# Kernel tuning notes

Hardware: AMD Instinct MI355X
Metric: run time of the kernel (lower is better)

Reference implementation:

```python
import jax, jax.numpy as jnp
import numpy as np

N = 50000
E = 800000
DIN = 64
DOUT = 64
H = 4
C = DOUT // H
EPS = 1e-5


def setup_inputs() -> dict:
    key = jax.random.key(0)
    ks = jax.random.split(key, 40)
    inp = {}
    inp["x"] = jax.random.normal(ks[0], (N, DIN), jnp.float32)
    inp["edge_index"] = jax.random.randint(ks[1], (2, E), 0, N, dtype=jnp.int32)
    inp["edge_weight"] = jax.random.uniform(ks[2], (E,), jnp.float32)
    inp["edge_attr"] = jax.random.normal(ks[3], (E, 1), jnp.float32)
    k = 4
    for i in range(2):
        din = DIN if i == 0 else DOUT
        s = din ** -0.5
        inp[f"gcn_w{i}"] = jax.random.normal(ks[k], (din, DOUT), jnp.float32) * s; k += 1
        inp[f"gcn_b{i}"] = jnp.zeros((DOUT,), jnp.float32)
        inp[f"res_w{i}"] = jax.random.normal(ks[k], (din, DOUT), jnp.float32) * s; k += 1
        inp[f"res_b{i}"] = jnp.zeros((DOUT,), jnp.float32)
        inp[f"ln_g{i}"] = jnp.ones((DOUT,), jnp.float32)
        inp[f"ln_b{i}"] = jnp.zeros((DOUT,), jnp.float32)
        sg = DOUT ** -0.5
        inp[f"gat_w{i}"] = jax.random.normal(ks[k], (DOUT, H * C), jnp.float32) * sg; k += 1
        inp[f"gat_b{i}"] = jnp.zeros((H * C,), jnp.float32)
        inp[f"att_src{i}"] = jax.random.normal(ks[k], (H, C), jnp.float32) * (C ** -0.5); k += 1
        inp[f"att_dst{i}"] = jax.random.normal(ks[k], (H, C), jnp.float32) * (C ** -0.5); k += 1
        inp[f"att_e{i}"] = jax.random.normal(ks[k], (H, C), jnp.float32) * (C ** -0.5); k += 1
        inp[f"ew_w{i}"] = jax.random.normal(ks[k], (1, H * C), jnp.float32); k += 1
    return inp


def _gcn(x, src0, dst0, ew, W, b):
    n = x.shape[0]
    sl = jnp.arange(n, dtype=src0.dtype)
    src = jnp.concatenate([src0, sl])
    dst = jnp.concatenate([dst0, sl])
    w = jnp.concatenate([ew, jnp.ones((n,), ew.dtype)])  # self-loop weight 1
    deg = jax.ops.segment_sum(w, dst, num_segments=n)
    dinv = jnp.where(deg > 0, jax.lax.rsqrt(deg), 0.0)
    norm = dinv[src] * w * dinv[dst]
    h = x @ W  # [n, DOUT]
    out = jax.ops.segment_sum(h[src] * norm[:, None], dst, num_segments=n)
    return out + b


def _gat(x, src0, dst0, ea, W, b, a_src, a_dst, a_e, We):
    n = x.shape[0]
    sl = jnp.arange(n, dtype=src0.dtype)
    src = jnp.concatenate([src0, sl])
    dst = jnp.concatenate([dst0, sl])
    loop_attr = jnp.broadcast_to(ea.mean(axis=0, keepdims=True), (n, ea.shape[1]))
    ea2 = jnp.concatenate([ea, loop_attr], axis=0)  # fill_value='mean'
    xl = (x @ W).reshape(n, H, C)
    a_s = (xl * a_src).sum(-1)  # [n,H]
    a_d = (xl * a_dst).sum(-1)
    a_ee = ((ea2 @ We).reshape(-1, H, C) * a_e).sum(-1)  # [E2,H]
    alpha = jax.nn.leaky_relu(a_s[src] + a_d[dst] + a_ee, 0.2)
    m = jax.ops.segment_max(alpha, dst, num_segments=n)
    e = jnp.exp(alpha - m[dst])
    s = jax.ops.segment_sum(e, dst, num_segments=n)
    alpha = e / (s[dst] + 1e-16)
    out = jax.ops.segment_sum(xl[src] * alpha[:, :, None], dst, num_segments=n)
    return out.reshape(n, H * C) + b


def _ln(x, g, b):
    mu = x.mean(-1, keepdims=True)
    v = ((x - mu) ** 2).mean(-1, keepdims=True)
    return (x - mu) * jax.lax.rsqrt(v + EPS) * g + b


def reference(x, edge_index, edge_weight, edge_attr,
              gcn_w0, gcn_b0, res_w0, res_b0, ln_g0, ln_b0,
              gat_w0, gat_b0, att_src0, att_dst0, att_e0, ew_w0,
              gcn_w1, gcn_b1, res_w1, res_b1, ln_g1, ln_b1,
              gat_w1, gat_b1, att_src1, att_dst1, att_e1, ew_w1):
    src0, dst0 = edge_index[0], edge_index[1]
    layers = [
        (gcn_w0, gcn_b0, res_w0, res_b0, ln_g0, ln_b0, gat_w0, gat_b0, att_src0, att_dst0, att_e0, ew_w0),
        (gcn_w1, gcn_b1, res_w1, res_b1, ln_g1, ln_b1, gat_w1, gat_b1, att_src1, att_dst1, att_e1, ew_w1),
    ]
    for (gw, gb, rw, rb, lg, lb, Wg, bg, a_s, a_d, a_e, We) in layers:
        residual = x @ rw + rb
        x = jax.nn.silu(_gcn(x, src0, dst0, edge_weight, gw, gb)) + residual
        x = _ln(x, lg, lb)
        x = jax.nn.silu(_gat(x, src0, dst0, edge_attr, Wg, bg, a_s, a_d, a_e, We)) + x
    return x  # down_sample=False -> Identity
```

## Files before the change

### kernel.cpp

```cpp
#include <hip/hip_runtime.h>
#include <hip/hip_fp16.h>

#define NN 50000
#define NE 800000
#define D 64
#define EPS 1e-5f
#define NT 3125
#define NB1 250
#define EPB 3200
#define NBIN 196
#define STOT 49152
#define SBLK 192
#define CAP 5888

typedef unsigned short ushort_t;
typedef unsigned int uint_t;
typedef __attribute__((ext_vector_type(8))) short bf16x8;
typedef __attribute__((ext_vector_type(4))) float f32x4;

__device__ __forceinline__ float wave_sum64(float v) {
#pragma unroll
  for (int m = 1; m <= 32; m <<= 1) v += __shfl_xor(v, m, 64);
  return v;
}
__device__ __forceinline__ float half_sum32(float v) {
#pragma unroll
  for (int m = 1; m <= 16; m <<= 1) v += __shfl_xor(v, m, 64);
  return v;
}
__device__ __forceinline__ float group_sum16(float v) {
#pragma unroll
  for (int m = 1; m <= 8; m <<= 1) v += __shfl_xor(v, m, 64);
  return v;
}
__device__ __forceinline__ float silu_f(float v) { return v / (1.f + __expf(-v)); }
__device__ __forceinline__ float lrelu_f(float v) { return v >= 0.f ? v : 0.2f * v; }
__device__ __forceinline__ ushort_t f2b(float x) {
  unsigned u = __float_as_uint(x);
  return (ushort_t)((u + 0x7FFFu + ((u >> 16) & 1u)) >> 16);
}
__device__ __forceinline__ float b2f(ushort_t u) {
  return __uint_as_float(((unsigned)u) << 16);
}
__device__ __forceinline__ float b2f_lo(uint_t u) {
  return __uint_as_float(u << 16);
}
__device__ __forceinline__ float b2f_hi(uint_t u) {
  return __uint_as_float(u & 0xFFFF0000u);
}
__device__ __forceinline__ ushort_t f2h(float x) {
  return __half_as_ushort(__float2half_rn(x));
}
__device__ __forceinline__ float h2f(unsigned u) {
  return __half2float(__ushort_as_half((ushort_t)(u & 0xFFFFu)));
}
__device__ __forceinline__ float sel4(float a, float b, float c, float d, int h) {
  float ab = (h & 1) ? b : a;
  float cd = (h & 1) ? d : c;
  return (h & 2) ? cd : ab;
}
__device__ __forceinline__ bf16x8 pack8(float4 a, float4 b) {
  bf16x8 r;
  r[0] = (short)f2b(a.x); r[1] = (short)f2b(a.y);
  r[2] = (short)f2b(a.z); r[3] = (short)f2b(a.w);
  r[4] = (short)f2b(b.x); r[5] = (short)f2b(b.y);
  r[6] = (short)f2b(b.z); r[7] = (short)f2b(b.w);
  return r;
}

__global__ void __launch_bounds__(256) k_hist(const int* __restrict__ ei,
                                              int* __restrict__ histG) {
  __shared__ int h[NBIN];
  int blk = blockIdx.x;
  for (int j = threadIdx.x; j < NBIN; j += 256) h[j] = 0;
  __syncthreads();
  int e0 = blk * EPB;
  for (int e = e0 + threadIdx.x; e < e0 + EPB; e += 256)
    atomicAdd(&h[ei[NE + e] >> 8], 1);
  __syncthreads();
  for (int j = threadIdx.x; j < NBIN; j += 256) histG[j * NB1 + blk] = h[j];
}

__global__ void __launch_bounds__(256) k_scanA(
    int* __restrict__ histG, int* __restrict__ bsum, float* __restrict__ scal,
    const float* __restrict__ Wg0, const float* __restrict__ Wg1,
    const float* __restrict__ W11, const float* __restrict__ W21,
    const float* __restrict__ We0, const float* __restrict__ ae0,
    const float* __restrict__ We1, const float* __restrict__ ae1,
    ushort_t* __restrict__ wg16, ushort_t* __restrict__ wd16,
    float* __restrict__ wea2) {
  if (blockIdx.x == SBLK) {
    int tid = threadIdx.x;
    for (int t = tid; t < 1024; t += 256) scal[t] = 0.f;
    for (int e = tid; e < 4096; e += 256) {
      int f = e >> 9, r = e & 511;
      int lane = r >> 3, j = r & 7;
      int s = (f >> 2) & 1, t = f & 3;
      int k = s * 32 + (lane >> 4) * 8 + j;
      int n = t * 16 + (lane & 15);
      wg16[e] = f2b(Wg0[k * D + n]);
      wg16[4096 + e] = f2b(Wg1[k * D + n]);
    }
    for (int e = tid; e < 8192; e += 256) {
      int f = e >> 9, r = e & 511;
      int lane = r >> 3, j = r & 7;
      int m = f >> 3, s = (f >> 2) & 1, t = f & 3;
      int k = s * 32 + (lane >> 4) * 8 + j;
      int n = t * 16 + (lane & 15);
      const float* Wm = m ? W21 : W11;
      wd16[e] = f2b(Wm[k * D + n]);
    }
    if (tid < 64) {
      float v = group_sum16(We0[tid] * ae0[tid]);
      if ((tid & 15) == 0) wea2[tid >> 4] = v;
    } else if (tid < 128) {
      int c = tid - 64;
      float v = group_sum16(We1[c] * ae1[c]);
      if ((c & 15) == 0) wea2[4 + (c >> 4)] = v;
    }
    return;
  }
  __shared__ int sm[256];
  int j = threadIdx.x;
  int i = blockIdx.x * 256 + j;
  const int TOT = NBIN * NB1;
  int v = (i < TOT) ? histG[i] : 0;
  sm[j] = v;
  __syncthreads();
  for (int off = 1; off < 256; off <<= 1) {
    int t = (j >= off) ? sm[j - off] : 0;
    __syncthreads();
    sm[j] += t;
    __syncthreads();
  }
  if (i < TOT) histG[i] = sm[j] - v;
  if (j == 255) bsum[blockIdx.x] = sm[255];
}

__global__ void __launch_bounds__(256) k_part(
    const int* __restrict__ ei, const float* __restrict__ ew,
    const float* __restrict__ ea, const int* __restrict__ histG,
    const int* __restrict__ bsum,
    uint2* __restrict__ rectmp, float* __restrict__ scal) {
  __shared__ int cur[NBIN];
  __shared__ int pex[256];
  int blk = blockIdx.x;
  int t = threadIdx.x;
  int v0 = (t < SBLK) ? bsum[t] : 0;
  pex[t] = v0;
  __syncthreads();
  for (int off = 1; off < 256; off <<= 1) {
    int u = (t >= off) ? pex[t - off] : 0;
    __syncthreads();
    pex[t] += u;
    __syncthreads();
  }
  int ex0 = pex[t] - v0;
  __syncthreads();
  pex[t] = ex0;
  __syncthreads();
  for (int j = t; j < NBIN; j += 256) {
    int idx = j * NB1 + blk;
    cur[j] = histG[idx] + pex[idx >> 8];
  }
  __syncthreads();
  int e0 = blk * EPB;
  float asum = 0.f;
  for (int e = e0 + t; e < e0 + EPB; e += 256) {
    int src = ei[e];
    int dst = ei[NE + e];
    float w = ew[e];
    float a = ea[e];
    asum += a;
    int slot = atomicAdd(&cur[dst >> 8], 1);
    uint2 r;
    r.x = (uint_t)(src & 0xFFFF) | ((uint_t)f2h(w) << 16);
    r.y = (uint_t)(dst & 0xFF) | ((uint_t)f2h(a) << 16);
    rectmp[slot] = r;
  }
  float s = wave_sum64(asum);
  if ((t & 63) == 0) {
    int slot = (blk * 4 + (t >> 6)) & 63;
    atomicAdd(&scal[(size_t)slot * 16], s);
  }
}

__global__ void __launch_bounds__(256) k_sfing(
    const uint2* __restrict__ rectmp, const int* __restrict__ histG,
    const int* __restrict__ bsum,
    uint_t* __restrict__ recw, uint_t* __restrict__ reca, int* __restrict__ rs,
    float* __restrict__ dinv, float* __restrict__ scal,
    const float* __restrict__ x, const float* __restrict__ W1,
    const float* __restrict__ W2, const float* __restrict__ b2,
    ushort_t* __restrict__ out1, float* __restrict__ out2) {
  __shared__ __align__(16) char smem[4096 + CAP * 8];
  int t = threadIdx.x;
  if (blockIdx.x >= NBIN) {
    ushort_t* wf = (ushort_t*)smem;
    for (int e = t; e < 8192; e += 256) {
      int f = e >> 9, r = e & 511;
      int lane = r >> 3, j = r & 7;
      int m = f >> 3, s = (f >> 2) & 1, tt = f & 3;
      int k = s * 32 + (lane >> 4) * 8 + j;
      int n = tt * 16 + (lane & 15);
      const float* Wm = m ? W2 : W1;
      wf[e] = f2b(Wm[k * D + n]);
    }
    __syncthreads();
    int tile = (blockIdx.x - NBIN) * 4 + (t >> 6);
    if (tile >= NT) return;
    int l = t & 63;
    int q = l >> 4, cn = l & 15;
    const float* xr = x + ((size_t)tile * 16 + cn) * D + q * 8;
    float4 xa = *(const float4*)xr;
    float4 xb = *(const float4*)(xr + 4);
    float4 xc = *(const float4*)(xr + 32);
    float4 xd = *(const float4*)(xr + 36);
    bf16x8 a0 = pack8(xa, xb), a1 = pack8(xc, xd);
    f32x4 acc1[4], acc2[4];
#pragma unroll
    for (int tt = 0; tt < 4; ++tt) {
      bf16x8 b10 = *(const bf16x8*)&wf[(0 * 8 + 0 * 4 + tt) * 512 + l * 8];
      bf16x8 b11 = *(const bf16x8*)&wf[(0 * 8 + 1 * 4 + tt) * 512 + l * 8];
      bf16x8 b20 = *(const bf16x8*)&wf[(1 * 8 + 0 * 4 + tt) * 512 + l * 8];
      bf16x8 b21 = *(const bf16x8*)&wf[(1 * 8 + 1 * 4 + tt) * 512 + l * 8];
      f32x4 z = {0.f, 0.f, 0.f, 0.f};
      acc1[tt] = __builtin_amdgcn_mfma_f32_16x16x32_bf16(a0, b10, z, 0, 0, 0);
      acc1[tt] = __builtin_amdgcn_mfma_f32_16x16x32_bf16(a1, b11, acc1[tt], 0, 0, 0);
      acc2[tt] = __builtin_amdgcn_mfma_f32_16x16x32_bf16(a0, b20, z, 0, 0, 0);
      acc2[tt] = __builtin_amdgcn_mfma_f32_16x16x32_bf16(a1, b21, acc2[tt], 0, 0, 0);
    }
#pragma unroll
    for (int tt = 0; tt < 4; ++tt) {
      float bb = b2[tt * 16 + cn];
#pragma unroll
      for (int r = 0; r < 4; ++r) {
        size_t row = (size_t)tile * 16 + q * 4 + r;
        out1[row * D + tt * 16 + cn] = f2b(acc1[tt][r]);
        out2[row * D + tt * 16 + cn] = acc2[tt][r] + bb;
      }
    }
    return;
  }
  int* cnt = (int*)smem;
  int* sc  = cnt + 256;
  int* cur = sc + 256;
  float* wsum = (float*)(cur + 256);
  uint2* lrec = (uint2*)(smem + 4096);
  int b = blockIdx.x;
  int v0 = (t < SBLK) ? bsum[t] : 0;
  sc[t] = v0;
  __syncthreads();
  for (int off = 1; off < 256; off <<= 1) {
    int u = (t >= off) ? sc[t - off] : 0;
    __syncthreads();
    sc[t] += u;
    __syncthreads();
  }
  int ex0 = sc[t] - v0;
  __syncthreads();
  sc[t] = ex0;
  __syncthreads();
  int i0 = b * NB1;
  int lo = histG[i0] + sc[i0 >> 8];
  int hi;
  if (b == NBIN - 1) {
    hi = NE;
  } else {
    int i1 = (b + 1) * NB1;
    hi = histG[i1] + sc[i1 >> 8];
  }
  __syncthreads();
  cnt[t] = 0;
  wsum[t] = 0.f;
  __syncthreads();
  int nc = min(hi - lo, CAP);
  for (int e = t; e < nc; e += 256) lrec[e] = rectmp[lo + e];
  __syncthreads();
  for (int e = t; e < nc; e += 256)
    atomicAdd(&cnt[lrec[e].y & 0xFFu], 1);
  for (int e = lo + CAP + t; e < hi; e += 256)
    atomicAdd(&cnt[rectmp[e].y & 0xFFu], 1);
  __syncthreads();
  int v = cnt[t];
  sc[t] = v;
  __syncthreads();
  for (int off = 1; off < 256; off <<= 1) {
    int u = (t >= off) ? sc[t - off] : 0;
    __syncthreads();
    sc[t] += u;
    __syncthreads();
  }
  int ex = sc[t] - v;
  int node = b * 256 + t;
  if (node < NN) rs[node] = lo + ex;
  if (b == NBIN - 1 && t == 0) rs[NN] = NE;
  cur[t] = lo + ex;
  __syncthreads();
  for (int e = t; e < nc; e += 256) {
    uint2 r = lrec[e];
    int dl = (int)(r.y & 0xFFu);
    int slot = atomicAdd(&cur[dl], 1);
    atomicAdd(&wsum[dl], h2f(r.x >> 16));
    uint_t src = r.x & 0xFFFFu;
    recw[slot] = r.x;
    reca[slot] = src | (r.y & 0xFFFF0000u);
  }
  for (int e = lo + CAP + t; e < hi; e += 256) {
    uint2 r = rectmp[e];
    int dl = (int)(r.y & 0xFFu);
    int slot = atomicAdd(&cur[dl], 1);
    atomicAdd(&wsum[dl], h2f(r.x >> 16));
    uint_t src = r.x & 0xFFFFu;
    recw[slot] = r.x;
    reca[slot] = src | (r.y & 0xFFFF0000u);
  }
  __syncthreads();
  if (node < NN) dinv[node] = rsqrtf(1.f + wsum[t]);
  if (b == 0 && t == 0) {
    float s = 0.f;
    for (int j = 0; j < 64; ++j) s += scal[(size_t)j * 16];
    scal[1] = s / (float)NE;
  }
}

__global__ void __launch_bounds__(256) k_gcn_gat(
    const ushort_t* __restrict__ h16, const float* __restrict__ res,
    const float* __restrict__ dinv, const int* __restrict__ rs,
    const uint_t* __restrict__ recw,
    const float* __restrict__ gb, const float* __restrict__ lg,
    const float* __restrict__ lb,
    const ushort_t* __restrict__ wg, const float* __restrict__ att_src,
    const float* __restrict__ att_dst,
    float* __restrict__ x2, ushort_t* __restrict__ xl,
    float* __restrict__ a_s, float* __restrict__ a_d) {
  __shared__ int ss[4][64];
  __shared__ float swt[4][64];
  __shared__ __align__(16) ushort_t xt[16][72];
  int w = threadIdx.x >> 6;
  int l = threadIdx.x & 63;
  int base = blockIdx.x * 8;
  int half = l >> 5, c = l & 31;
  int iA = base + 2 * w;
  int iB = iA + 1;
  int i = iA + half;
  float di = dinv[i];
  uint_t u0 = *(const uint_t*)&h16[(size_t)i * D + 2 * c];
  float dii = di * di;
  float acc0 = dii * b2f_lo(u0);
  float acc1 = dii * b2f_hi(u0);
  int kA = rs[iA], kA1 = rs[iA + 1];
  int kB = rs[iB], kB1 = rs[iB + 1];
  int sbase = half * 32;
  while (kA < kA1 || kB < kB1) {
    int cntA = min(32, kA1 - kA);
    int cntB = min(32, kB1 - kB);
    int myk = half ? kB : kA;
    int mycnt = half ? cntB : cntA;
    int src = 0; float wn = 0.f;
    if (c < mycnt) {
      uint_t r = recw[(size_t)(myk + c)];
      src = (int)(r & 0xFFFFu);
      wn = dinv[src] * h2f(r >> 16) * di;
    }
    ss[w][l] = src;
    swt[w][l] = wn;
    int nm = max(cntA, cntB);
    int j = 0;
    for (; j + 4 <= nm; j += 4) {
      int4 s4 = *(const int4*)&ss[w][sbase + j];
      float4 w4 = *(const float4*)&swt[w][sbase + j];
      uint_t ua = *(const uint_t*)&h16[(size_t)s4.x * D + 2 * c];
      uint_t ub = *(const uint_t*)&h16[(size_t)s4.y * D + 2 * c];
      uint_t uc = *(const uint_t*)&h16[(size_t)s4.z * D + 2 * c];
      uint_t ud = *(const uint_t*)&h16[(size_t)s4.w * D + 2 * c];
      acc0 = fmaf(w4.x, b2f_lo(ua), acc0); acc1 = fmaf(w4.x, b2f_hi(ua), acc1);
      acc0 = fmaf(w4.y, b2f_lo(ub), acc0); acc1 = fmaf(w4.y, b2f_hi(ub), acc1);
      acc0 = fmaf(w4.z, b2f_lo(uc), acc0); acc1 = fmaf(w4.z, b2f_hi(uc), acc1);
      acc0 = fmaf(w4.w, b2f_lo(ud), acc0); acc1 = fmaf(w4.w, b2f_hi(ud), acc1);
    }
    for (; j < nm; ++j) {
      int s1 = ss[w][sbase + j];
      float w1 = swt[w][sbase + j];
      uint_t u = *(const uint_t*)&h16[(size_t)s1 * D + 2 * c];
      acc0 = fmaf(w1, b2f_lo(u), acc0);
      acc1 = fmaf(w1, b2f_hi(u), acc1);
    }
    kA += cntA; kB += cntB;
  }
  float2 gb2 = *(const float2*)&gb[2 * c];
  float2 lg2 = *(const float2*)&lg[2 * c];
  float2 lb2 = *(const float2*)&lb[2 * c];
  float2 rs2 = *(const float2*)&res[(size_t)i * D + 2 * c];
  float x0 = silu_f(acc0 + gb2.x) + rs2.x;
  float x1 = silu_f(acc1 + gb2.y) + rs2.y;
  float mu = half_sum32(x0 + x1) * (1.f / 64.f);
  float d0 = x0 - mu, d1 = x1 - mu;
  float var = half_sum32(d0 * d0 + d1 * d1) * (1.f / 64.f);
  float rinv = rsqrtf(var + EPS);
  float o0 = d0 * rinv * lg2.x + lb2.x;
  float o1 = d1 * rinv * lg2.y + lb2.y;
  float2 o2; o2.x = o0; o2.y = o1;
  *(float2*)&x2[(size_t)i * D + 2 * c] = o2;
  uint_t pk = (uint_t)f2b(o0) | ((uint_t)f2b(o1) << 16);
  *(uint_t*)&xt[2 * w + half][2 * c] = pk;
  {
    ushort_t* xz = &xt[8][0];
    for (int e = threadIdx.x; e < 8 * 72; e += 256) xz[e] = 0;
  }
  __syncthreads();
  int t = w;
  int q = l >> 4, cn = l & 15;
  bf16x8 a0 = *(const bf16x8*)&xt[cn][q * 8];
  bf16x8 a1 = *(const bf16x8*)&xt[cn][q * 8 + 32];
  bf16x8 b0 = *(const bf16x8*)&wg[(size_t)((0 * 4 + t) * 512 + l * 8)];
  bf16x8 b1 = *(const bf16x8*)&wg[(size_t)((1 * 4 + t) * 512 + l * 8)];
  f32x4 z = {0.f, 0.f, 0.f, 0.f};
  f32x4 acc = __builtin_amdgcn_mfma_f32_16x16x32_bf16(a0, b0, z, 0, 0, 0);
  acc = __builtin_amdgcn_mfma_f32_16x16x32_bf16(a1, b1, acc, 0, 0, 0);
  if (q < 2) {
    float av = att_src[t * 16 + cn];
    float dv = att_dst[t * 16 + cn];
#pragma unroll
    for (int r = 0; r < 4; ++r) {
      size_t row = (size_t)base + q * 4 + r;
      xl[row * D + t * 16 + cn] = f2b(acc[r]);
      float vs = group_sum16(acc[r] * av);
      float vd = group_sum16(acc[r] * dv);
      if (cn == 0) {
        a_s[row * 4 + t] = vs;
        a_d[row * 4 + t] = vd;
      }
    }
  }
}

template <int FUSE>
__global__ void __launch_bounds__(256) k_gat_fin(
    const ushort_t* __restrict__ xl16, const float* __restrict__ x2,
    const float* __restrict__ a_s, const float* __restrict__ a_d,
    const int* __restrict__ rs, const uint_t* __restrict__ reca,
    const float* __restrict__ wea, const float* __restrict__ scal,
    const float* __restrict__ bg,
    const ushort_t* __restrict__ wd, const float* __restrict__ b2,
    ushort_t* __restrict__ out1, float* __restrict__ out2,
    float* __restrict__ xout) {
  __shared__ int ss[4][64];
  __shared__ float el[4][4][68];
  __shared__ __align__(16) ushort_t xt[16][72];
  int w = threadIdx.x >> 6;
  int l = threadIdx.x & 63;
  int base = blockIdx.x * 8;
  int half = l >> 5, c = l & 31;
  int iA = base + 2 * w;
  int iB = iA + 1;
  int i = iA + half;
  int hh = c >> 3;
  float4 wv4 = *(const float4*)wea;
  float mean_attr = scal[1];
  float we_h = sel4(wv4.x, wv4.y, wv4.z, wv4.w, hh);
  float ad_h = a_d[(size_t)i * 4 + hh];
  float as_i = a_s[(size_t)i * 4 + hh];
  float eS = __expf(lrelu_f(as_i + ad_h + mean_attr * we_h));
  float s = eS;
  uint_t u0 = *(const uint_t*)&xl16[(size_t)i * D + 2 * c];
  float acc0 = eS * b2f_lo(u0);
  float acc1 = eS * b2f_hi(u0);
  float4 ad4 = *(const float4*)(a_d + (size_t)i * 4);
  int kA = rs[iA], kA1 = rs[iA + 1];
  int kB = rs[iB], kB1 = rs[iB + 1];
  int sbase = half * 32;
  while (kA < kA1 || kB < kB1) {
    int cntA = min(32, kA1 - kA);
    int cntB = min(32, kB1 - kB);
    int myk = half ? kB : kA;
    int mycnt = half ? cntB : cntA;
    int src = 0;
    float e0v = 0.f, e1v = 0.f, e2v = 0.f, e3v = 0.f;
    if (c < mycnt) {
      uint_t r = reca[(size_t)(myk + c)];
      src = (int)(r & 0xFFFFu);
      float ea = h2f(r >> 16);
      float4 as4 = *(const float4*)(a_s + (size_t)src * 4);
      e0v = __expf(lrelu_f(as4.x + fmaf(ea, wv4.x, ad4.x)));
      e1v = __expf(lrelu_f(as4.y + fmaf(ea, wv4.y, ad4.y)));
      e2v = __expf(lrelu_f(as4.z + fmaf(ea, wv4.z, ad4.z)));
      e3v = __expf(lrelu_f(as4.w + fmaf(ea, wv4.w, ad4.w)));
    }
    ss[w][l] = src;
    el[w][0][l] = e0v;
    el[w][1][l] = e1v;
    el[w][2][l] = e2v;
    el[w][3][l] = e3v;
    int nm = max(cntA, cntB);
    int j = 0;
    for (; j + 4 <= nm; j += 4) {
      int4 s4 = *(const int4*)&ss[w][sbase + j];
      float4 e4 = *(const float4*)&el[w][hh][sbase + j];
      uint_t ua = *(const uint_t*)&xl16[(size_t)s4.x * D + 2 * c];
      uint_t ub = *(const uint_t*)&xl16[(size_t)s4.y * D + 2 * c];
      uint_t uc = *(const uint_t*)&xl16[(size_t)s4.z * D + 2 * c];
      uint_t ud = *(const uint_t*)&xl16[(size_t)s4.w * D + 2 * c];
      acc0 = fmaf(e4.x, b2f_lo(ua), acc0); acc1 = fmaf(e4.x, b2f_hi(ua), acc1);
      acc0 = fmaf(e4.y, b2f_lo(ub), acc0); acc1 = fmaf(e4.y, b2f_hi(ub), acc1);
      acc0 = fmaf(e4.z, b2f_lo(uc), acc0); acc1 = fmaf(e4.z, b2f_hi(uc), acc1);
      acc0 = fmaf(e4.w, b2f_lo(ud), acc0); acc1 = fmaf(e4.w, b2f_hi(ud), acc1);
      s += (e4.x + e4.y) + (e4.z + e4.w);
    }
    for (; j < nm; ++j) {
      int s1 = ss[w][sbase + j];
      float e1 = el[w][hh][sbase + j];
      uint_t u = *(const uint_t*)&xl16[(size_t)s1 * D + 2 * c];
      acc0 = fmaf(e1, b2f_lo(u), acc0);
      acc1 = fmaf(e1, b2f_hi(u), acc1);
      s += e1;
    }
    kA += cntA; kB += cntB;
  }
  float2 bg2 = *(const float2*)&bg[2 * c];
  float rcp = 1.f / (s + 1e-16f);
  float o0 = acc0 * rcp + bg2.x;
  float o1 = acc1 * rcp + bg2.y;
  float2 x22 = *(const float2*)&x2[(size_t)i * D + 2 * c];
  float v0 = silu_f(o0) + x22.x;
  float v1 = silu_f(o1) + x22.y;
  if (FUSE) {
    uint_t pk = (uint_t)f2b(v0) | ((uint_t)f2b(v1) << 16);
    *(uint_t*)&xt[2 * w + half][2 * c] = pk;
    {
      ushort_t* xz = &xt[8][0];
      for (int e = threadIdx.x; e < 8 * 72; e += 256) xz[e] = 0;
    }
    __syncthreads();
    int t = w;
    int q = l >> 4, cn = l & 15;
    bf16x8 a0 = *(const bf16x8*)&xt[cn][q * 8];
    bf16x8 a1 = *(const bf16x8*)&xt[cn][q * 8 + 32];
#pragma unroll
    for (int m = 0; m < 2; ++m) {
      bf16x8 b0 = *(const bf16x8*)&wd[(size_t)((m * 8 + 0 * 4 + t) * 512 + l * 8)];
      bf16x8 b1 = *(const bf16x8*)&wd[(size_t)((m * 8 + 1 * 4 + t) * 512 + l * 8)];
      f32x4 z = {0.f, 0.f, 0.f, 0.f};
      f32x4 acc = __builtin_amdgcn_mfma_f32_16x16x32_bf16(a0, b0, z, 0, 0, 0);
      acc = __builtin_amdgcn_mfma_f32_16x16x32_bf16(a1, b1, acc, 0, 0, 0);
      if (q < 2) {
        float bb = (m == 1) ? b2[t * 16 + cn] : 0.f;
#pragma unroll
        for (int r = 0; r < 4; ++r) {
          size_t row = (size_t)base + q * 4 + r;
          if (m == 0)
            out1[row * D + t * 16 + cn] = f2b(acc[r]);
          else
            out2[row * D + t * 16 + cn] = acc[r] + bb;
        }
      }
    }
  } else {
    float2 v2; v2.x = v0; v2.y = v1;
    *(float2*)&xout[(size_t)i * D + 2 * c] = v2;
  }
}


extern "C" void kernel_launch(void* const* d_in, const int* in_sizes, int n_in,
                              void* d_out, int out_size, void* d_ws, size_t ws_size,
                              hipStream_t stream) {
  (void)in_sizes; (void)n_in; (void)out_size; (void)ws_size;
  const float* x  = (const float*)d_in[0];
  const int*   ei = (const int*)d_in[1];
  const float* ew = (const float*)d_in[2];
  const float* ea = (const float*)d_in[3];
  const float* P[2][12];
  for (int l = 0; l < 2; ++l)
    for (int j = 0; j < 12; ++j) P[l][j] = (const float*)d_in[4 + l * 12 + j];

  float* W = (float*)d_ws;
  const size_t o_rs    = 0;
  const size_t o_dinv  = o_rs + NN + 16;
  const size_t o_wea   = o_dinv + NN;
  const size_t o_scal  = o_wea + 16;
  const size_t o_bsum  = o_scal + 1024;
  const size_t o_hist  = o_bsum + 256;
  const size_t o_recw  = o_hist + STOT;
  const size_t o_reca  = o_recw + NE;
  const size_t o_rtmp  = o_reca + NE;
  const size_t o_h16   = o_rtmp + (size_t)NE * 2;
  const size_t o_xl16  = o_h16 + (size_t)NN * D / 2;
  const size_t o_res   = o_xl16 + (size_t)NN * D / 2;
  const size_t o_x2    = o_res + (size_t)NN * D;
  const size_t o_as    = o_x2 + (size_t)NN * D;
  const size_t o_ad    = o_as + (size_t)NN * 4;
  const size_t o_wg16  = o_ad + (size_t)NN * 4;
  const size_t o_wd16  = o_wg16 + 4096;

  int*      rs    = (int*)(W + o_rs);
  float*    dinv  = W + o_dinv;
  float*    wea2  = W + o_wea;
  float*    scal  = W + o_scal;
  int*      bsum  = (int*)(W + o_bsum);
  int*      histG = (int*)(W + o_hist);
  uint_t*   recw  = (uint_t*)(W + o_recw);
  uint_t*   reca  = (uint_t*)(W + o_reca);
  uint2*    rtmp  = (uint2*)(W + o_rtmp);
  ushort_t* h16   = (ushort_t*)(W + o_h16);
  ushort_t* xl16  = (ushort_t*)(W + o_xl16);
  float*    resb  = W + o_res;
  float*    x2b   = W + o_x2;
  float*    asb   = W + o_as;
  float*    adb   = W + o_ad;
  ushort_t* wg16  = (ushort_t*)(W + o_wg16);
  ushort_t* wd16  = (ushort_t*)(W + o_wd16);

  const int B = 256;
  const int gSf = NBIN + (NT + 3) / 4;
  const int gN2 = NN / 8;

  k_hist<<<NB1, B, 0, stream>>>(ei, histG);
  k_scanA<<<SBLK + 1, B, 0, stream>>>(histG, bsum, scal,
                                      P[0][6], P[1][6], P[1][0], P[1][2],
                                      P[0][11], P[0][10], P[1][11], P[1][10],
                                      wg16, wd16, wea2);
  k_part<<<NB1, B, 0, stream>>>(ei, ew, ea, histG, bsum, rtmp, scal);
  k_sfing<<<gSf, B, 0, stream>>>(rtmp, histG, bsum, recw, reca, rs, dinv, scal,
                                 x, P[0][0], P[0][2], P[0][3], h16, resb);

  k_gcn_gat<<<gN2, B, 0, stream>>>(h16, resb, dinv, rs, recw,
                                   P[0][1], P[0][4], P[0][5],
                                   wg16, P[0][8], P[0][9],
                                   x2b, xl16, asb, adb);
  k_gat_fin<1><<<gN2, B, 0, stream>>>(xl16, x2b, asb, adb, rs, reca,
                                      wea2, scal, P[0][7],
                                      wd16, P[1][3], h16, resb, nullptr);
  k_gcn_gat<<<gN2, B, 0, stream>>>(h16, resb, dinv, rs, recw,
                                   P[1][1], P[1][4], P[1][5],
                                   wg16 + 4096, P[1][8], P[1][9],
                                   x2b, xl16, asb, adb);
  k_gat_fin<0><<<gN2, B, 0, stream>>>(xl16, x2b, asb, adb, rs, reca,
                                      wea2 + 4, scal, P[1][7],
                                      nullptr, nullptr, nullptr, nullptr,
                                      (float*)d_out);
}
```

Before: 277.2 us.

## Split edge gathers across two 16-lane groups with 8-byte loads, cache GCN norms

The GCN and GAT aggregation loops now have each 32-lane half-wave split into two 16-lane groups. Each group handles alternate edges and gathers 4 bf16 features per lane with 8-byte loads, and the two partial sums are combined with a shuffle at the end. This doubles the edges in flight per wave and widens each gather, aiming to hide irregular-gather latency better. Layer 0 also writes per-edge GCN normalisation weights into a new buffer that layer 1 reads back, skipping the dinv[src] gather. Source attention scores are additionally stored as fp16 to halve the per-edge gather size, at the cost of a small loss of precision.

```diff
diff --git a/kernel.cpp b/kernel.cpp
--- a/kernel.cpp
+++ b/kernel.cpp
@@ -21,11 +21,6 @@
 __device__ __forceinline__ float wave_sum64(float v) {
 #pragma unroll
   for (int m = 1; m <= 32; m <<= 1) v += __shfl_xor(v, m, 64);
-  return v;
-}
-__device__ __forceinline__ float half_sum32(float v) {
-#pragma unroll
-  for (int m = 1; m <= 16; m <<= 1) v += __shfl_xor(v, m, 64);
   return v;
 }
 __device__ __forceinline__ float group_sum16(float v) {
@@ -324,86 +319,109 @@
   }
 }
 
+template <int LAYER>
 __global__ void __launch_bounds__(256) k_gcn_gat(
     const ushort_t* __restrict__ h16, const float* __restrict__ res,
     const float* __restrict__ dinv, const int* __restrict__ rs,
-    const uint_t* __restrict__ recw,
+    const uint_t* __restrict__ recw, float* __restrict__ normc,
     const float* __restrict__ gb, const float* __restrict__ lg,
     const float* __restrict__ lb,
     const ushort_t* __restrict__ wg, const float* __restrict__ att_src,
     const float* __restrict__ att_dst,
     float* __restrict__ x2, ushort_t* __restrict__ xl,
-    float* __restrict__ a_s, float* __restrict__ a_d) {
+    float* __restrict__ a_s, float* __restrict__ a_d,
+    ushort_t* __restrict__ asf16) {
   __shared__ int ss[4][64];
   __shared__ float swt[4][64];
   __shared__ __align__(16) ushort_t xt[16][72];
   int w = threadIdx.x >> 6;
   int l = threadIdx.x & 63;
   int base = blockIdx.x * 8;
-  int half = l >> 5, c = l & 31;
+  int half = l >> 5;
+  int p = (l >> 4) & 1;
+  int cc = l & 15;
+  int ce = l & 31;
   int iA = base + 2 * w;
   int iB = iA + 1;
   int i = iA + half;
   float di = dinv[i];
-  uint_t u0 = *(const uint_t*)&h16[(size_t)i * D + 2 * c];
-  float dii = di * di;
-  float acc0 = dii * b2f_lo(u0);
-  float acc1 = dii * b2f_hi(u0);
+  float dii = (p == 0) ? di * di : 0.f;
+  uint2 u0 = *(const uint2*)&h16[(size_t)i * D + 4 * cc];
+  float a0c = dii * b2f_lo(u0.x);
+  float a1c = dii * b2f_hi(u0.x);
+  float a2c = dii * b2f_lo(u0.y);
+  float a3c = dii * b2f_hi(u0.y);
   int kA = rs[iA], kA1 = rs[iA + 1];
   int kB = rs[iB], kB1 = rs[iB + 1];
   int sbase = half * 32;
+  int gbase = sbase + (p << 4);
   while (kA < kA1 || kB < kB1) {
     int cntA = min(32, kA1 - kA);
     int cntB = min(32, kB1 - kB);
     int myk = half ? kB : kA;
     int mycnt = half ? cntB : cntA;
     int src = 0; float wn = 0.f;
-    if (c < mycnt) {
-      uint_t r = recw[(size_t)(myk + c)];
+    if (ce < mycnt) {
+      uint_t r = recw[(size_t)(myk + ce)];
       src = (int)(r & 0xFFFFu);
-      wn = dinv[src] * h2f(r >> 16) * di;
-    }
-    ss[w][l] = src;
-    swt[w][l] = wn;
+      if (LAYER == 0) {
+        wn = dinv[src] * h2f(r >> 16) * di;
+        normc[(size_t)(myk + ce)] = wn;
+      } else {
+        wn = normc[(size_t)(myk + ce)];
+      }
+    }
+    int slot = sbase + ((ce & 1) << 4) + (ce >> 1);
+    ss[w][slot] = src;
+    swt[w][slot] = wn;
     int nm = max(cntA, cntB);
-    int j = 0;
-    for (; j + 4 <= nm; j += 4) {
-      int4 s4 = *(const int4*)&ss[w][sbase + j];
-      float4 w4 = *(const float4*)&swt[w][sbase + j];
-      uint_t ua = *(const uint_t*)&h16[(size_t)s4.x * D + 2 * c];
-      uint_t ub = *(const uint_t*)&h16[(size_t)s4.y * D + 2 * c];
-      uint_t uc = *(const uint_t*)&h16[(size_t)s4.z * D + 2 * c];
-      uint_t ud = *(const uint_t*)&h16[(size_t)s4.w * D + 2 * c];
-      acc0 = fmaf(w4.x, b2f_lo(ua), acc0); acc1 = fmaf(w4.x, b2f_hi(ua), acc1);
-      acc0 = fmaf(w4.y, b2f_lo(ub), acc0); acc1 = fmaf(w4.y, b2f_hi(ub), acc1);
-      acc0 = fmaf(w4.z, b2f_lo(uc), acc0); acc1 = fmaf(w4.z, b2f_hi(uc), acc1);
-      acc0 = fmaf(w4.w, b2f_lo(ud), acc0); acc1 = fmaf(w4.w, b2f_hi(ud), acc1);
-    }
-    for (; j < nm; ++j) {
-      int s1 = ss[w][sbase + j];
-      float w1 = swt[w][sbase + j];
-      uint_t u = *(const uint_t*)&h16[(size_t)s1 * D + 2 * c];
-      acc0 = fmaf(w1, b2f_lo(u), acc0);
-      acc1 = fmaf(w1, b2f_hi(u), acc1);
+    int npj = (nm + 1) >> 1;
+    for (int pj = 0; pj < npj; pj += 4) {
+      int4 s4 = *(const int4*)&ss[w][gbase + pj];
+      float4 w4 = *(const float4*)&swt[w][gbase + pj];
+      uint2 ua = *(const uint2*)&h16[(size_t)s4.x * D + 4 * cc];
+      uint2 ub = *(const uint2*)&h16[(size_t)s4.y * D + 4 * cc];
+      uint2 uc = *(const uint2*)&h16[(size_t)s4.z * D + 4 * cc];
+      uint2 ud = *(const uint2*)&h16[(size_t)s4.w * D + 4 * cc];
+      a0c = fmaf(w4.x, b2f_lo(ua.x), a0c); a1c = fmaf(w4.x, b2f_hi(ua.x), a1c);
+      a2c = fmaf(w4.x, b2f_lo(ua.y), a2c); a3c = fmaf(w4.x, b2f_hi(ua.y), a3c);
+      a0c = fmaf(w4.y, b2f_lo(ub.x), a0c); a1c = fmaf(w4.y, b2f_hi(ub.x), a1c);
+      a2c = fmaf(w4.y, b2f_lo(ub.y), a2c); a3c = fmaf(w4.y, b2f_hi(ub.y), a3c);
+      a0c = fmaf(w4.z, b2f_lo(uc.x), a0c); a1c = fmaf(w4.z, b2f_hi(uc.x), a1c);
+      a2c = fmaf(w4.z, b2f_lo(uc.y), a2c); a3c = fmaf(w4.z, b2f_hi(uc.y), a3c);
+      a0c = fmaf(w4.w, b2f_lo(ud.x), a0c); a1c = fmaf(w4.w, b2f_hi(ud.x), a1c);
+      a2c = fmaf(w4.w, b2f_lo(ud.y), a2c); a3c = fmaf(w4.w, b2f_hi(ud.y), a3c);
     }
     kA += cntA; kB += cntB;
   }
-  float2 gb2 = *(const float2*)&gb[2 * c];
-  float2 lg2 = *(const float2*)&lg[2 * c];
-  float2 lb2 = *(const float2*)&lb[2 * c];
-  float2 rs2 = *(const float2*)&res[(size_t)i * D + 2 * c];
-  float x0 = silu_f(acc0 + gb2.x) + rs2.x;
-  float x1 = silu_f(acc1 + gb2.y) + rs2.y;
-  float mu = half_sum32(x0 + x1) * (1.f / 64.f);
-  float d0 = x0 - mu, d1 = x1 - mu;
-  float var = half_sum32(d0 * d0 + d1 * d1) * (1.f / 64.f);
+  a0c += __shfl_xor(a0c, 16, 64);
+  a1c += __shfl_xor(a1c, 16, 64);
+  a2c += __shfl_xor(a2c, 16, 64);
+  a3c += __shfl_xor(a3c, 16, 64);
+  float4 gb4 = *(const float4*)&gb[4 * cc];
+  float4 lg4 = *(const float4*)&lg[4 * cc];
+  float4 lb4 = *(const float4*)&lb[4 * cc];
+  float4 rs4 = *(const float4*)&res[(size_t)i * D + 4 * cc];
+  float x0 = silu_f(a0c + gb4.x) + rs4.x;
+  float x1 = silu_f(a1c + gb4.y) + rs4.y;
+  float x2v = silu_f(a2c + gb4.z) + rs4.z;
+  float x3 = silu_f(a3c + gb4.w) + rs4.w;
+  float mu = group_sum16((x0 + x1) + (x2v + x3)) * (1.f / 64.f);
+  float d0 = x0 - mu, d1 = x1 - mu, d2 = x2v - mu, d3 = x3 - mu;
+  float var = group_sum16((d0 * d0 + d1 * d1) + (d2 * d2 + d3 * d3)) * (1.f / 64.f);
   float rinv = rsqrtf(var + EPS);
-  float o0 = d0 * rinv * lg2.x + lb2.x;
-  float o1 = d1 * rinv * lg2.y + lb2.y;
-  float2 o2; o2.x = o0; o2.y = o1;
-  *(float2*)&x2[(size_t)i * D + 2 * c] = o2;
-  uint_t pk = (uint_t)f2b(o0) | ((uint_t)f2b(o1) << 16);
-  *(uint_t*)&xt[2 * w + half][2 * c] = pk;
+  float o0 = d0 * rinv * lg4.x + lb4.x;
+  float o1 = d1 * rinv * lg4.y + lb4.y;
+  float o2 = d2 * rinv * lg4.z + lb4.z;
+  float o3 = d3 * rinv * lg4.w + lb4.w;
+  if (p == 0) {
+    float4 ov; ov.x = o0; ov.y = o1; ov.z = o2; ov.w = o3;
+    *(float4*)&x2[(size_t)i * D + 4 * cc] = ov;
+    uint2 pk;
+    pk.x = (uint_t)f2b(o0) | ((uint_t)f2b(o1) << 16);
+    pk.y = (uint_t)f2b(o2) | ((uint_t)f2b(o3) << 16);
+    *(uint2*)&xt[2 * w + half][4 * cc] = pk;
+  }
   {
     ushort_t* xz = &xt[8][0];
     for (int e = threadIdx.x; e < 8 * 72; e += 256) xz[e] = 0;
@@ -411,13 +429,13 @@
   __syncthreads();
   int t = w;
   int q = l >> 4, cn = l & 15;
-  bf16x8 a0 = *(const bf16x8*)&xt[cn][q * 8];
-  bf16x8 a1 = *(const bf16x8*)&xt[cn][q * 8 + 32];
-  bf16x8 b0 = *(const bf16x8*)&wg[(size_t)((0 * 4 + t) * 512 + l * 8)];
-  bf16x8 b1 = *(const bf16x8*)&wg[(size_t)((1 * 4 + t) * 512 + l * 8)];
+  bf16x8 fa0 = *(const bf16x8*)&xt[cn][q * 8];
+  bf16x8 fa1 = *(const bf16x8*)&xt[cn][q * 8 + 32];
+  bf16x8 fb0 = *(const bf16x8*)&wg[(size_t)((0 * 4 + t) * 512 + l * 8)];
+  bf16x8 fb1 = *(const bf16x8*)&wg[(size_t)((1 * 4 + t) * 512 + l * 8)];
   f32x4 z = {0.f, 0.f, 0.f, 0.f};
-  f32x4 acc = __builtin_amdgcn_mfma_f32_16x16x32_bf16(a0, b0, z, 0, 0, 0);
-  acc = __builtin_amdgcn_mfma_f32_16x16x32_bf16(a1, b1, acc, 0, 0, 0);
+  f32x4 acc = __builtin_amdgcn_mfma_f32_16x16x32_bf16(fa0, fb0, z, 0, 0, 0);
+  acc = __builtin_amdgcn_mfma_f32_16x16x32_bf16(fa1, fb1, acc, 0, 0, 0);
   if (q < 2) {
     float av = att_src[t * 16 + cn];
     float dv = att_dst[t * 16 + cn];
@@ -430,6 +448,7 @@
       if (cn == 0) {
         a_s[row * 4 + t] = vs;
         a_d[row * 4 + t] = vd;
+        asf16[row * 4 + t] = f2h(vs);
       }
     }
   }
@@ -439,6 +458,7 @@
 __global__ void __launch_bounds__(256) k_gat_fin(
     const ushort_t* __restrict__ xl16, const float* __restrict__ x2,
     const float* __restrict__ a_s, const float* __restrict__ a_d,
+    const ushort_t* __restrict__ asf16,
     const int* __restrict__ rs, const uint_t* __restrict__ reca,
     const float* __restrict__ wea, const float* __restrict__ scal,
     const float* __restrict__ bg,
@@ -451,25 +471,32 @@
   int w = threadIdx.x >> 6;
   int l = threadIdx.x & 63;
   int base = blockIdx.x * 8;
-  int half = l >> 5, c = l & 31;
+  int half = l >> 5;
+  int p = (l >> 4) & 1;
+  int cc = l & 15;
+  int ce = l & 31;
   int iA = base + 2 * w;
   int iB = iA + 1;
   int i = iA + half;
-  int hh = c >> 3;
+  int hh = cc >> 2;
   float4 wv4 = *(const float4*)wea;
   float mean_attr = scal[1];
   float we_h = sel4(wv4.x, wv4.y, wv4.z, wv4.w, hh);
   float ad_h = a_d[(size_t)i * 4 + hh];
   float as_i = a_s[(size_t)i * 4 + hh];
   float eS = __expf(lrelu_f(as_i + ad_h + mean_attr * we_h));
-  float s = eS;
-  uint_t u0 = *(const uint_t*)&xl16[(size_t)i * D + 2 * c];
-  float acc0 = eS * b2f_lo(u0);
-  float acc1 = eS * b2f_hi(u0);
+  float eSm = (p == 0) ? eS : 0.f;
+  float s = eSm;
+  uint2 u0 = *(const uint2*)&xl16[(size_t)i * D + 4 * cc];
+  float a0c = eSm * b2f_lo(u0.x);
+  float a1c = eSm * b2f_hi(u0.x);
+  float a2c = eSm * b2f_lo(u0.y);
+  float a3c = eSm * b2f_hi(u0.y);
   float4 ad4 = *(const float4*)(a_d + (size_t)i * 4);
   int kA = rs[iA], kA1 = rs[iA + 1];
   int kB = rs[iB], kB1 = rs[iB + 1];
   int sbase = half * 32;
+  int gbase = sbase + (p << 4);
   while (kA < kA1 || kB < kB1) {
     int cntA = min(32, kA1 - kA);
     int cntB = min(32, kB1 - kB);
@@ -477,56 +504,64 @@
     int mycnt = half ? cntB : cntA;
     int src = 0;
     float e0v = 0.f, e1v = 0.f, e2v = 0.f, e3v = 0.f;
-    if (c < mycnt) {
-      uint_t r = reca[(size_t)(myk + c)];
+    if (ce < mycnt) {
+      uint_t r = reca[(size_t)(myk + ce)];
       src = (int)(r & 0xFFFFu);
       float ea = h2f(r >> 16);
-      float4 as4 = *(const float4*)(a_s + (size_t)src * 4);
-      e0v = __expf(lrelu_f(as4.x + fmaf(ea, wv4.x, ad4.x)));
-      e1v = __expf(lrelu_f(as4.y + fmaf(ea, wv4.y, ad4.y)));
-      e2v = __expf(lrelu_f(as4.z + fmaf(ea, wv4.z, ad4.z)));
-      e3v = __expf(lrelu_f(as4.w + fmaf(ea, wv4.w, ad4.w)));
-    }
-    ss[w][l] = src;
-    el[w][0][l] = e0v;
-    el[w][1][l] = e1v;
-    el[w][2][l] = e2v;
-    el[w][3][l] = e3v;
+      uint2 au = *(const uint2*)&asf16[(size_t)src * 4];
+      float as0 = h2f(au.x), as1 = h2f(au.x >> 16);
+      float as2 = h2f(au.y), as3 = h2f(au.y >> 16);
+      e0v = __expf(lrelu_f(as0 + fmaf(ea, wv4.x, ad4.x)));
+      e1v = __expf(lrelu_f(as1 + fmaf(ea, wv4.y, ad4.y)));
+      e2v = __expf(lrelu_f(as2 + fmaf(ea, wv4.z, ad4.z)));
+      e3v = __expf(lrelu_f(as3 + fmaf(ea, wv4.w, ad4.w)));
+    }
+    int slot = sbase + ((ce & 1) << 4) + (ce >> 1);
+    ss[w][slot] = src;
+    el[w][0][slot] = e0v;
+    el[w][1][slot] = e1v;
+    el[w][2][slot] = e2v;
+    el[w][3][slot] = e3v;
     int nm = max(cntA, cntB);
-    int j = 0;
-    for (; j + 4 <= nm; j += 4) {
-      int4 s4 = *(const int4*)&ss[w][sbase + j];
-      float4 e4 = *(const float4*)&el[w][hh][sbase + j];
-      uint_t ua = *(const uint_t*)&xl16[(size_t)s4.x * D + 2 * c];
-      uint_t ub = *(const uint_t*)&xl16[(size_t)s4.y * D + 2 * c];
-      uint_t uc = *(const uint_t*)&xl16[(size_t)s4.z * D + 2 * c];
-      uint_t ud = *(const uint_t*)&xl16[(size_t)s4.w * D + 2 * c];
-      acc0 = fmaf(e4.x, b2f_lo(ua), acc0); acc1 = fmaf(e4.x, b2f_hi(ua), acc1);
-      acc0 = fmaf(e4.y, b2f_lo(ub), acc0); acc1 = fmaf(e4.y, b2f_hi(ub), acc1);
-      acc0 = fmaf(e4.z, b2f_lo(uc), acc0); acc1 = fmaf(e4.z, b2f_hi(uc), acc1);
-      acc0 = fmaf(e4.w, b2f_lo(ud), acc0); acc1 = fmaf(e4.w, b2f_hi(ud), acc1);
+    int npj = (nm + 1) >> 1;
+    for (int pj = 0; pj < npj; pj += 4) {
+      int4 s4 = *(const int4*)&ss[w][gbase + pj];
+      float4 e4 = *(const float4*)&el[w][hh][gbase + pj];
+      uint2 ua = *(const uint2*)&xl16[(size_t)s4.x * D + 4 * cc];
+      uint2 ub = *(const uint2*)&xl16[(size_t)s4.y * D + 4 * cc];
+      uint2 uc = *(const uint2*)&xl16[(size_t)s4.z * D + 4 * cc];
+      uint2 ud = *(const uint2*)&xl16[(size_t)s4.w * D + 4 * cc];
+      a0c = fmaf(e4.x, b2f_lo(ua.x), a0c); a1c = fmaf(e4.x, b2f_hi(ua.x), a1c);
+      a2c = fmaf(e4.x, b2f_lo(ua.y), a2c); a3c = fmaf(e4.x, b2f_hi(ua.y), a3c);
+      a0c = fmaf(e4.y, b2f_lo(ub.x), a0c); a1c = fmaf(e4.y, b2f_hi(ub.x), a1c);
+      a2c = fmaf(e4.y, b2f_lo(ub.y), a2c); a3c = fmaf(e4.y, b2f_hi(ub.y), a3c);
+      a0c = fmaf(e4.z, b2f_lo(uc.x), a0c); a1c = fmaf(e4.z, b2f_hi(uc.x), a1c);
+      a2c = fmaf(e4.z, b2f_lo(uc.y), a2c); a3c = fmaf(e4.z, b2f_hi(uc.y), a3c);
+      a0c = fmaf(e4.w, b2f_lo(ud.x), a0c); a1c = fmaf(e4.w, b2f_hi(ud.x), a1c);
+      a2c = fmaf(e4.w, b2f_lo(ud.y), a2c); a3c = fmaf(e4.w, b2f_hi(ud.y), a3c);
       s += (e4.x + e4.y) + (e4.z + e4.w);
     }
-    for (; j < nm; ++j) {
-      int s1 = ss[w][sbase + j];
-      float e1 = el[w][hh][sbase + j];
-      uint_t u = *(const uint_t*)&xl16[(size_t)s1 * D + 2 * c];
-      acc0 = fmaf(e1, b2f_lo(u), acc0);
-      acc1 = fmaf(e1, b2f_hi(u), acc1);
-      s += e1;
-    }
     kA += cntA; kB += cntB;
   }
-  float2 bg2 = *(const float2*)&bg[2 * c];
+  a0c += __shfl_xor(a0c, 16, 64);
+  a1c += __shfl_xor(a1c, 16, 64);
+  a2c += __shfl_xor(a2c, 16, 64);
+  a3c += __shfl_xor(a3c, 16, 64);
+  s += __shfl_xor(s, 16, 64);
+  float4 bg4 = *(const float4*)&bg[4 * cc];
   float rcp = 1.f / (s + 1e-16f);
-  float o0 = acc0 * rcp + bg2.x;
-  float o1 = acc1 * rcp + bg2.y;
-  float2 x22 = *(const float2*)&x2[(size_t)i * D + 2 * c];
-  float v0 = silu_f(o0) + x22.x;
-  float v1 = silu_f(o1) + x22.y;
+  float4 x24 = *(const float4*)&x2[(size_t)i * D + 4 * cc];
+  float v0 = silu_f(a0c * rcp + bg4.x) + x24.x;
+  float v1 = silu_f(a1c * rcp + bg4.y) + x24.y;
+  float v2 = silu_f(a2c * rcp + bg4.z) + x24.z;
+  float v3 = silu_f(a3c * rcp + bg4.w) + x24.w;
   if (FUSE) {
-    uint_t pk = (uint_t)f2b(v0) | ((uint_t)f2b(v1) << 16);
-    *(uint_t*)&xt[2 * w + half][2 * c] = pk;
+    if (p == 0) {
+      uint2 pk;
+      pk.x = (uint_t)f2b(v0) | ((uint_t)f2b(v1) << 16);
+      pk.y = (uint_t)f2b(v2) | ((uint_t)f2b(v3) << 16);
+      *(uint2*)&xt[2 * w + half][4 * cc] = pk;
+    }
     {
       ushort_t* xz = &xt[8][0];
       for (int e = threadIdx.x; e < 8 * 72; e += 256) xz[e] = 0;
@@ -534,15 +569,15 @@
     __syncthreads();
     int t = w;
     int q = l >> 4, cn = l & 15;
-    bf16x8 a0 = *(const bf16x8*)&xt[cn][q * 8];
-    bf16x8 a1 = *(const bf16x8*)&xt[cn][q * 8 + 32];
+    bf16x8 fa0 = *(const bf16x8*)&xt[cn][q * 8];
+    bf16x8 fa1 = *(const bf16x8*)&xt[cn][q * 8 + 32];
 #pragma unroll
     for (int m = 0; m < 2; ++m) {
-      bf16x8 b0 = *(const bf16x8*)&wd[(size_t)((m * 8 + 0 * 4 + t) * 512 + l * 8)];
-      bf16x8 b1 = *(const bf16x8*)&wd[(size_t)((m * 8 + 1 * 4 + t) * 512 + l * 8)];
+      bf16x8 fb0 = *(const bf16x8*)&wd[(size_t)((m * 8 + 0 * 4 + t) * 512 + l * 8)];
+      bf16x8 fb1 = *(const bf16x8*)&wd[(size_t)((m * 8 + 1 * 4 + t) * 512 + l * 8)];
       f32x4 z = {0.f, 0.f, 0.f, 0.f};
-      f32x4 acc = __builtin_amdgcn_mfma_f32_16x16x32_bf16(a0, b0, z, 0, 0, 0);
-      acc = __builtin_amdgcn_mfma_f32_16x16x32_bf16(a1, b1, acc, 0, 0, 0);
+      f32x4 acc = __builtin_amdgcn_mfma_f32_16x16x32_bf16(fa0, fb0, z, 0, 0, 0);
+      acc = __builtin_amdgcn_mfma_f32_16x16x32_bf16(fa1, fb1, acc, 0, 0, 0);
       if (q < 2) {
         float bb = (m == 1) ? b2[t * 16 + cn] : 0.f;
 #pragma unroll
@@ -556,8 +591,10 @@
       }
     }
   } else {
-    float2 v2; v2.x = v0; v2.y = v1;
-    *(float2*)&xout[(size_t)i * D + 2 * c] = v2;
+    if (p == 0) {
+      float4 vv; vv.x = v0; vv.y = v1; vv.z = v2; vv.w = v3;
+      *(float4*)&xout[(size_t)i * D + 4 * cc] = vv;
+    }
   }
 }
 
@@ -583,14 +620,16 @@
   const size_t o_hist  = o_bsum + 256;
   const size_t o_recw  = o_hist + STOT;
   const size_t o_reca  = o_recw + NE;
-  const size_t o_rtmp  = o_reca + NE;
+  const size_t o_norm  = o_reca + NE;
+  const size_t o_rtmp  = o_norm + NE;
   const size_t o_h16   = o_rtmp + (size_t)NE * 2;
   const size_t o_xl16  = o_h16 + (size_t)NN * D / 2;
   const size_t o_res   = o_xl16 + (size_t)NN * D / 2;
   const size_t o_x2    = o_res + (size_t)NN * D;
   const size_t o_as    = o_x2 + (size_t)NN * D;
   const size_t o_ad    = o_as + (size_t)NN * 4;
-  const size_t o_wg16  = o_ad + (size_t)NN * 4;
+  const size_t o_ash   = o_ad + (size_t)NN * 4;
+  const size_t o_wg16  = o_ash + (size_t)NN * 2;
   const size_t o_wd16  = o_wg16 + 4096;
 
   int*      rs    = (int*)(W + o_rs);
@@ -601,6 +640,7 @@
   int*      histG = (int*)(W + o_hist);
   uint_t*   recw  = (uint_t*)(W + o_recw);
   uint_t*   reca  = (uint_t*)(W + o_reca);
+  float*    normc = W + o_norm;
   uint2*    rtmp  = (uint2*)(W + o_rtmp);
   ushort_t* h16   = (ushort_t*)(W + o_h16);
   ushort_t* xl16  = (ushort_t*)(W + o_xl16);
@@ -608,6 +648,7 @@
   float*    x2b   = W + o_x2;
   float*    asb   = W + o_as;
   float*    adb   = W + o_ad;
+  ushort_t* ashb  = (ushort_t*)(W + o_ash);
   ushort_t* wg16  = (ushort_t*)(W + o_wg16);
   ushort_t* wd16  = (ushort_t*)(W + o_wd16);
 
@@ -624,18 +665,18 @@
   k_sfing<<<gSf, B, 0, stream>>>(rtmp, histG, bsum, recw, reca, rs, dinv, scal,
                                  x, P[0][0], P[0][2], P[0][3], h16, resb);
 
-  k_gcn_gat<<<gN2, B, 0, stream>>>(h16, resb, dinv, rs, recw,
-                                   P[0][1], P[0][4], P[0][5],
-                                   wg16, P[0][8], P[0][9],
-                                   x2b, xl16, asb, adb);
-  k_gat_fin<1><<<gN2, B, 0, stream>>>(xl16, x2b, asb, adb, rs, reca,
+  k_gcn_gat<0><<<gN2, B, 0, stream>>>(h16, resb, dinv, rs, recw, normc,
+                                      P[0][1], P[0][4], P[0][5],
+                                      wg16, P[0][8], P[0][9],
+                                      x2b, xl16, asb, adb, ashb);
+  k_gat_fin<1><<<gN2, B, 0, stream>>>(xl16, x2b, asb, adb, ashb, rs, reca,
                                       wea2, scal, P[0][7],
                                       wd16, P[1][3], h16, resb, nullptr);
-  k_gcn_gat<<<gN2, B, 0, stream>>>(h16, resb, dinv, rs, recw,
-                                   P[1][1], P[1][4], P[1][5],
-                                   wg16 + 4096, P[1][8], P[1][9],
-                                   x2b, xl16, asb, adb);
-  k_gat_fin<0><<<gN2, B, 0, stream>>>(xl16, x2b, asb, adb, rs, reca,
+  k_gcn_gat<1><<<gN2, B, 0, stream>>>(h16, resb, dinv, rs, recw, normc,
+                                      P[1][1], P[1][4], P[1][5],
+                                      wg16 + 4096, P[1][8], P[1][9],
+                                      x2b, xl16, asb, adb, ashb);
+  k_gat_fin<0><<<gN2, B, 0, stream>>>(xl16, x2b, asb, adb, ashb, rs, reca,
                                       wea2 + 4, scal, P[1][7],
                                       nullptr, nullptr, nullptr, nullptr,
                                       (float*)d_out);
```

Result: no change. 272.9 us (-1.5%).
